# Kernel optimization log

Hardware: AMD Instinct MI355X
Metric: run time of the kernel (lower is better)

## Reference

```python
import jax, jax.numpy as jnp
import numpy as np

B, T, IN, H, L = 256, 80, 39, 256, 5


def _xavier(key, shape):
    fan_out, fan_in = shape[0], shape[1]
    std = (2.0 / (fan_in + fan_out)) ** 0.5
    return std * jax.random.normal(key, shape, dtype=jnp.float32)


def setup_inputs() -> dict:
    key = jax.random.key(0)
    ks = jax.random.split(key, 4 + 2 * L)
    x = jax.random.normal(ks[0], (B, T, IN), dtype=jnp.float32)
    # PyTorch LSTM params, gate order (i, f, g, o); biases zero per init.
    W_ih0 = _xavier(ks[1], (4 * H, IN))                       # layer 0 input weights
    W_ih_rest = jnp.stack([_xavier(ks[2 + l], (4 * H, H)) for l in range(L - 1)])  # [L-1,4H,H]
    W_hh = jnp.stack([_xavier(ks[1 + L + l], (4 * H, H)) for l in range(L)])       # [L,4H,H]
    b_ih = jnp.zeros((L, 4 * H), dtype=jnp.float32)
    b_hh = jnp.zeros((L, 4 * H), dtype=jnp.float32)
    fc_w = _xavier(ks[2 * L + 1], (1, H))
    fc_b = jnp.zeros((1,), dtype=jnp.float32)
    return {"x": x, "W_ih0": W_ih0, "W_ih_rest": W_ih_rest, "W_hh": W_hh,
            "b_ih": b_ih, "b_hh": b_hh, "fc_w": fc_w, "fc_b": fc_b}


def _lstm_layer(xs, W_ih, W_hh_l, b_ih_l, b_hh_l):
    # xs: [B,T,D]. Precompute input projection for all timesteps (one big GEMM).
    x_proj = jnp.einsum('btd,gd->btg', xs, W_ih) + b_ih_l + b_hh_l  # [B,T,4H]

    def step(carry, xp):
        h, c = carry
        gates = xp + h @ W_hh_l.T                 # [B,4H]
        i, f, g, o = jnp.split(gates, 4, axis=-1)
        c = jax.nn.sigmoid(f) * c + jax.nn.sigmoid(i) * jnp.tanh(g)
        h = jax.nn.sigmoid(o) * jnp.tanh(c)
        return (h, c), h

    b = xs.shape[0]
    h0 = jnp.zeros((b, H), dtype=xs.dtype)
    _, hs = jax.lax.scan(step, (h0, h0), jnp.swapaxes(x_proj, 0, 1))
    return jnp.swapaxes(hs, 0, 1)  # [B,T,H]


def reference(x, W_ih0, W_ih_rest, W_hh, b_ih, b_hh, fc_w, fc_b):
    h = _lstm_layer(x, W_ih0, W_hh[0], b_ih[0], b_hh[0])
    for l in range(1, L):
        h = _lstm_layer(h, W_ih_rest[l - 1], W_hh[l], b_ih[l], b_hh[l])
    out = jnp.einsum('bth,oh->bto', h, fc_w) + fc_b  # [B,T,1]
    return out[..., 0]  # [B,T]
```

## Files before the change

kernel.cpp:

```cpp
#include <hip/hip_runtime.h>

#define B_ 256
#define T_ 80
#define IN_ 39
#define H_ 256
#define G_ 1024
#define L_ 5
#define TC_ 16
#define NCH_ 5

#define XP_FLOATS   (B_ * TC_ * G_)
#define HBUF_FLOATS (B_ * T_ * H_)
#define CBUF_FLOATS (B_ * H_)
#define WG_FLOATS   (L_ * G_ * H_)
#define HX_FLOATS   (2 * 32 * 2048)
#define FLG_INTS_L  2048

#define AG __HIP_MEMORY_SCOPE_AGENT
#define WGS __HIP_MEMORY_SCOPE_WORKGROUP

__device__ __forceinline__ float sigm(float x) { return 1.0f / (1.0f + expf(-x)); }
__device__ __forceinline__ void fma4(float4& a, float s, const float4& w) {
    a.x = fmaf(s, w.x, a.x); a.y = fmaf(s, w.y, a.y);
    a.z = fmaf(s, w.z, a.z); a.w = fmaf(s, w.w, a.w);
}
__device__ __forceinline__ void red4(float4& a) {
    a.x += __shfl_xor(a.x, 32); a.y += __shfl_xor(a.y, 32);
    a.z += __shfl_xor(a.z, 32); a.w += __shfl_xor(a.w, 32);
}

__device__ __forceinline__ float4 ld_mall_16B(const float* p) {
    float4 v;
    asm volatile("global_load_dwordx4 %0, %1, off sc0 sc1\n\t"
                 "s_waitcnt vmcnt(0)"
                 : "=&v"(v) : "v"(p) : "memory");
    return v;
}

__device__ __forceinline__ void cbar(int* cnt, int& seq) {
    seq += 4;
    asm volatile("s_waitcnt lgkmcnt(0)" ::: "memory");
    if ((threadIdx.x & 63) == 0)
        __hip_atomic_fetch_add(cnt, 1, __ATOMIC_RELAXED, WGS);
    while (__hip_atomic_load(cnt, __ATOMIC_RELAXED, WGS) < seq)
        __builtin_amdgcn_s_sleep(1);
    asm volatile("s_waitcnt lgkmcnt(0)" ::: "memory");
}

extern "C" __global__ void __launch_bounds__(256)
wt_kernel(const float* __restrict__ Whh, float* __restrict__ Wg) {
    const int gid = blockIdx.x * 256 + threadIdx.x;
    const int g4 = gid & 3;
    const int j  = (gid >> 2) & 31;
    const int k  = (gid >> 7) & 255;
    const int s  = (gid >> 15) & 7;
    const int l  = gid >> 18;
    Wg[gid] = Whh[((size_t)(l * 1024 + g4 * 256 + s * 32 + j)) * 256 + k];
}

extern "C" __global__ void __launch_bounds__(256)
proj_multi(const float* __restrict__ x, const float* __restrict__ Wih0,
           const float* __restrict__ Wihr,
           const float* __restrict__ bih, const float* __restrict__ bhh,
           const float* __restrict__ hbuf,
           float* __restrict__ xp_base, unsigned long long xp_s,
           int d, int lmin) {
    __shared__ float As[16 * 132];
    __shared__ float Bs[16 * 68];
    const int task = blockIdx.x >> 9;
    const int l = lmin + task;
    const int ch = d - l;
    const int t0 = ch * TC_;
    const int K = (l == 0) ? IN_ : H_;
    const float* src = (l == 0) ? x : hbuf;
    const float* Wih = (l == 0) ? Wih0 : (Wihr + (size_t)(l - 1) * G_ * H_);
    const float* bihl = bih + l * G_;
    const float* bhhl = bhh + l * G_;
    float* xp = xp_base + (size_t)l * xp_s;

    const int bid9 = blockIdx.x & 511;
    const int tid = threadIdx.x;
    const int mt = bid9 >> 4, nt = bid9 & 15;
    const int tx = tid & 15, ty = tid >> 4;
    const int lrA = tid >> 1, lc8 = (tid & 1) * 8;
    const int lrB = tid >> 2, lc4 = (tid & 3) * 4;

    const int ar = mt * 128 + lrA;
    const int ab = ar >> 4;
    const int at = t0 + (ar & 15);
    const float* arow = src + ((size_t)ab * T_ + at) * K;
    const int brow_idx = (lrB & 3) * 256 + nt * 16 + (lrB >> 2);
    const float* brow = Wih + (size_t)brow_idx * K;

    float acc[8][4];
    #pragma unroll
    for (int i = 0; i < 8; ++i)
        #pragma unroll
        for (int j = 0; j < 4; ++j) acc[i][j] = 0.0f;

    for (int k0 = 0; k0 < K; k0 += 16) {
        __syncthreads();
        if (K == IN_) {
            #pragma unroll
            for (int i = 0; i < 8; ++i) {
                const int k = k0 + lc8 + i;
                As[(lc8 + i) * 132 + lrA] = (k < IN_) ? arow[k] : 0.0f;
            }
            #pragma unroll
            for (int i = 0; i < 4; ++i) {
                const int k = k0 + lc4 + i;
                Bs[(lc4 + i) * 68 + lrB] = (k < IN_) ? brow[k] : 0.0f;
            }
        } else {
            float4 a0 = *(const float4*)(arow + k0 + lc8);
            float4 a1 = *(const float4*)(arow + k0 + lc8 + 4);
            As[(lc8 + 0) * 132 + lrA] = a0.x;
            As[(lc8 + 1) * 132 + lrA] = a0.y;
            As[(lc8 + 2) * 132 + lrA] = a0.z;
            As[(lc8 + 3) * 132 + lrA] = a0.w;
            As[(lc8 + 4) * 132 + lrA] = a1.x;
            As[(lc8 + 5) * 132 + lrA] = a1.y;
            As[(lc8 + 6) * 132 + lrA] = a1.z;
            As[(lc8 + 7) * 132 + lrA] = a1.w;
            float4 bv = *(const float4*)(brow + k0 + lc4);
            Bs[(lc4 + 0) * 68 + lrB] = bv.x;
            Bs[(lc4 + 1) * 68 + lrB] = bv.y;
            Bs[(lc4 + 2) * 68 + lrB] = bv.z;
            Bs[(lc4 + 3) * 68 + lrB] = bv.w;
        }
        __syncthreads();
        #pragma unroll
        for (int kk = 0; kk < 16; ++kk) {
            const float4 aA = *(const float4*)&As[kk * 132 + ty * 8];
            const float4 aB = *(const float4*)&As[kk * 132 + ty * 8 + 4];
            const float4 b4 = *(const float4*)&Bs[kk * 68 + tx * 4];
            acc[0][0] += aA.x * b4.x; acc[0][1] += aA.x * b4.y;
            acc[0][2] += aA.x * b4.z; acc[0][3] += aA.x * b4.w;
            acc[1][0] += aA.y * b4.x; acc[1][1] += aA.y * b4.y;
            acc[1][2] += aA.y * b4.z; acc[1][3] += aA.y * b4.w;
            acc[2][0] += aA.z * b4.x; acc[2][1] += aA.z * b4.y;
            acc[2][2] += aA.z * b4.z; acc[2][3] += aA.z * b4.w;
            acc[3][0] += aA.w * b4.x; acc[3][1] += aA.w * b4.y;
            acc[3][2] += aA.w * b4.z; acc[3][3] += aA.w * b4.w;
            acc[4][0] += aB.x * b4.x; acc[4][1] += aB.x * b4.y;
            acc[4][2] += aB.x * b4.z; acc[4][3] += aB.x * b4.w;
            acc[5][0] += aB.y * b4.x; acc[5][1] += aB.y * b4.y;
            acc[5][2] += aB.y * b4.z; acc[5][3] += aB.y * b4.w;
            acc[6][0] += aB.z * b4.x; acc[6][1] += aB.z * b4.y;
            acc[6][2] += aB.z * b4.z; acc[6][3] += aB.z * b4.w;
            acc[7][0] += aB.w * b4.x; acc[7][1] += aB.w * b4.y;
            acc[7][2] += aB.w * b4.z; acc[7][3] += aB.w * b4.w;
        }
    }
    const int unit = nt * 16 + tx;
    const float bs0 = bihl[0 * 256 + unit] + bhhl[0 * 256 + unit];
    const float bs1 = bihl[1 * 256 + unit] + bhhl[1 * 256 + unit];
    const float bs2 = bihl[2 * 256 + unit] + bhhl[2 * 256 + unit];
    const float bs3 = bihl[3 * 256 + unit] + bhhl[3 * 256 + unit];
    #pragma unroll
    for (int i = 0; i < 8; ++i) {
        const int row = mt * 128 + ty * 8 + i;
        float4 o;
        o.x = acc[i][0] + bs0; o.y = acc[i][1] + bs1;
        o.z = acc[i][2] + bs2; o.w = acc[i][3] + bs3;
        *(float4*)&xp[(size_t)row * G_ + unit * 4] = o;
    }
}

extern "C" __global__ void __launch_bounds__(512, 2)
rec_multi(const float* __restrict__ xp_base, unsigned long long xp_s,
          const float* __restrict__ wg, float* __restrict__ hbuf,
          float* __restrict__ cbuf_base, unsigned long long cb_s,
          float* __restrict__ hx_base, unsigned long long hx_s,
          int* __restrict__ flg_base, unsigned long long flg_s,
          int d, int lmin) {
    __shared__ float sH[2048];
    __shared__ float sP[2 * 4 * 32 * 20];
    __shared__ int   barC[2];

    const int tid = threadIdx.x;
    const int task = blockIdx.x >> 8;
    const int l = lmin + task;
    const int ch = d - l;
    const int b8 = blockIdx.x & 255;
    const int grp = b8 >> 3;
    const int s   = b8 & 7;
    const int t0 = ch * TC_;
    const int chkb = (l * NCH_ + ch) * TC_;
    const int first = (ch == 0);

    const float* xp = xp_base + (size_t)l * xp_s;
    const float* Wg_l = wg + (size_t)l * (G_ * H_);
    float* cbuf = cbuf_base + (size_t)l * cb_s;
    float* hx = hx_base + (size_t)l * hx_s;
    int* flg = flg_base + (size_t)l * flg_s;

    const int c = tid >> 8;
    const int tp = tid & 255;
    const int jj = tp & 31;
    const int ks = tp >> 5;
    const int w4 = tp >> 6;
    const int fb2 = tp >> 5;
    const int unit = s * 32 + jj;
    const int bglob = grp * 8 + c * 4 + (fb2 & 3);
    float* sPc = sP + c * 2560;
    int* mycnt = barC + c;
    int* flgc = flg + (grp * 2 + c) * 32;

    if (tid < 2) barC[tid] = 0;

    const float4* Wg4 = (const float4*)Wg_l + (size_t)s * 8192;
    float4 wreg[32];
    #pragma unroll
    for (int kk = 0; kk < 32; ++kk)
        wreg[kk] = Wg4[(size_t)(ks * 32 + kk) * 32 + jj];

    float creg = 0.0f;
    if (tp < 128 && !first) creg = cbuf[(size_t)bglob * H_ + unit];

    __syncthreads();

    const float4* sH4 = (const float4*)sH;
    int seq = 0;

    for (int tt = 0; tt < TC_; ++tt) {
        const int t = t0 + tt;

        float4 xv = make_float4(0.f, 0.f, 0.f, 0.f);
        if (tp < 128)
            xv = *(const float4*)&xp[((size_t)bglob * TC_ + tt) * G_ + unit * 4];

        if (tt == 0 && first) {
            *(float4*)&sH[tp * 8 + c * 4] = make_float4(0.f, 0.f, 0.f, 0.f);
        } else {
            if ((tid & 63) < 8) {
                int* fp = flgc + (tid & 63);
                const int tgt = chkb + tt;
                while (__hip_atomic_load(fp, __ATOMIC_RELAXED, AG) < tgt)
                    __builtin_amdgcn_s_sleep(1);
            }
            const float* hsf = hx + (size_t)((((tt + 1) & 1)) * 32 + grp) * 2048
                                  + (size_t)tp * 8 + c * 4;
            *(float4*)&sH[tp * 8 + c * 4] = ld_mall_16B(hsf);
        }
        cbar(mycnt, seq);

        float4 a0 = {0,0,0,0}, a1 = {0,0,0,0}, a2 = {0,0,0,0}, a3 = {0,0,0,0};
        #pragma unroll
        for (int kk = 0; kk < 32; ++kk) {
            const int k = ks * 32 + kk;
            const float4 wv = wreg[kk];
            const float4 hc = sH4[k * 2 + c];
            fma4(a0, hc.x, wv); fma4(a1, hc.y, wv);
            fma4(a2, hc.z, wv); fma4(a3, hc.w, wv);
        }
        red4(a0); red4(a1); red4(a2); red4(a3);
        if ((tid & 63) < 32) {
            float4* pp = (float4*)&sPc[(w4 * 32 + jj) * 20];
            pp[0] = a0; pp[1] = a1; pp[2] = a2; pp[3] = a3;
        }
        cbar(mycnt, seq);

        if (tp < 128) {
            float4 g4 = xv;
            #pragma unroll
            for (int w2 = 0; w2 < 4; ++w2) {
                const float4 pw = *(const float4*)&sPc[(w2 * 32 + jj) * 20 + fb2 * 4];
                g4.x += pw.x; g4.y += pw.y; g4.z += pw.z; g4.w += pw.w;
            }
            const float I = sigm(g4.x);
            const float F = sigm(g4.y);
            const float Gt = tanhf(g4.z);
            const float O = sigm(g4.w);
            creg = F * creg + I * Gt;
            const float hval = O * tanhf(creg);
            hbuf[((size_t)bglob * T_ + t) * H_ + unit] = hval;

            const float hpart = __shfl_xor(hval, 32);
            if ((fb2 & 1) == 0) {
                const unsigned long long pv =
                    ((unsigned long long)__float_as_uint(hpart) << 32)
                    | __float_as_uint(hval);
                unsigned long long* dst = (unsigned long long*)
                    (hx + (size_t)((tt & 1) * 32 + grp) * 2048
                        + unit * 8 + c * 4 + fb2);
                __hip_atomic_store(dst, pv, __ATOMIC_RELAXED, AG);
            }
        }

        asm volatile("s_waitcnt vmcnt(0)" ::: "memory");
        cbar(mycnt, seq);
        if (tp == 0)
            __hip_atomic_store(flgc + s, chkb + tt + 1, __ATOMIC_RELAXED, AG);
    }

    if (tp < 128) cbuf[(size_t)bglob * H_ + unit] = creg;
}

extern "C" __global__ void __launch_bounds__(128)
fc_kernel(const float* __restrict__ hbuf, const float* __restrict__ fcw,
          const float* __restrict__ fcb, float* __restrict__ out) {
    __shared__ float wsm[256];
    const int tid = threadIdx.x;
    const int b = blockIdx.x;
    if (tid < 64) ((float4*)wsm)[tid] = ((const float4*)fcw)[tid];
    __syncthreads();
    if (tid < T_) {
        const float4* h4p = (const float4*)(hbuf + ((size_t)b * T_ + tid) * H_);
        const float4* w4p = (const float4*)wsm;
        float acc = fcb[0];
        #pragma unroll 8
        for (int k4 = 0; k4 < 64; ++k4) {
            float4 h4 = h4p[k4], w4 = w4p[k4];
            acc += h4.x * w4.x + h4.y * w4.y + h4.z * w4.z + h4.w * w4.w;
        }
        out[b * T_ + tid] = acc;
    }
}

extern "C" void kernel_launch(void* const* d_in, const int* in_sizes, int n_in,
                              void* d_out, int out_size, void* d_ws, size_t ws_size,
                              hipStream_t stream) {
    (void)in_sizes; (void)n_in; (void)out_size;
    const float* x    = (const float*)d_in[0];
    const float* Wih0 = (const float*)d_in[1];
    const float* Wihr = (const float*)d_in[2];
    const float* Whh  = (const float*)d_in[3];
    const float* bih  = (const float*)d_in[4];
    const float* bhh  = (const float*)d_in[5];
    const float* fcw  = (const float*)d_in[6];
    const float* fcb  = (const float*)d_in[7];
    float* out = (float*)d_out;
    float* ws  = (float*)d_ws;

    const size_t WF_ELEMS = (size_t)5 * XP_FLOATS + HBUF_FLOATS
                          + (size_t)5 * CBUF_FLOATS + WG_FLOATS
                          + (size_t)5 * HX_FLOATS + (size_t)5 * FLG_INTS_L;
    const int wf = (ws_size >= WF_ELEMS * 4) ? 1 : 0;

    const unsigned long long xp_s  = wf ? XP_FLOATS   : 0;
    const unsigned long long cb_s  = wf ? CBUF_FLOATS : 0;
    const unsigned long long hx_s  = wf ? HX_FLOATS   : 0;
    const unsigned long long flg_s = wf ? FLG_INTS_L  : 0;
    const int nrep = wf ? 5 : 1;

    float* xp   = ws;
    float* hbuf = xp + (size_t)nrep * XP_FLOATS;
    float* cbuf = hbuf + HBUF_FLOATS;
    float* wg   = cbuf + (size_t)nrep * CBUF_FLOATS;
    float* hx   = wg + WG_FLOATS;
    int*   flg  = (int*)(hx + (size_t)nrep * HX_FLOATS);

    hipMemsetAsync(flg, 0, (size_t)nrep * FLG_INTS_L * sizeof(int), stream);
    hipLaunchKernelGGL(wt_kernel, dim3(WG_FLOATS / 256), dim3(256), 0, stream, Whh, wg);

    if (wf) {
        for (int dd = 0; dd <= L_ + NCH_ - 2; ++dd) {
            const int lmin = (dd - (NCH_ - 1) > 0) ? (dd - (NCH_ - 1)) : 0;
            const int lmax = (dd < L_ - 1) ? dd : (L_ - 1);
            const int n = lmax - lmin + 1;
            hipLaunchKernelGGL(proj_multi, dim3(n * 512), dim3(256), 0, stream,
                               x, Wih0, Wihr, bih, bhh, hbuf, xp, xp_s, dd, lmin);
            hipLaunchKernelGGL(rec_multi, dim3(n * 256), dim3(512), 0, stream,
                               xp, xp_s, wg, hbuf, cbuf, cb_s, hx, hx_s,
                               flg, flg_s, dd, lmin);
        }
    } else {
        for (int l = 0; l < L_; ++l) {
            for (int ch = 0; ch < NCH_; ++ch) {
                const int dd = l + ch;
                hipLaunchKernelGGL(proj_multi, dim3(512), dim3(256), 0, stream,
                                   x, Wih0, Wihr, bih, bhh, hbuf, xp, xp_s, dd, l);
                hipLaunchKernelGGL(rec_multi, dim3(256), dim3(512), 0, stream,
                                   xp, xp_s, wg, hbuf, cbuf, cb_s, hx, hx_s,
                                   flg, flg_s, dd, l);
            }
        }
    }
    hipLaunchKernelGGL(fc_kernel, dim3(B_), dim3(128), 0, stream, hbuf, fcw, fcb, out);
}
```

Measured before the change: 2.172 ms.

## Replace diagonal wavefront with fixed two-task-per-launch layer/chunk schedule

The multi-layer wavefront used to launch every ready (layer, chunk) task on a diagonal together, up to five tasks and 1280 recurrence blocks at once. It now follows a hand-written 14-step schedule that launches at most two tasks per projection/recurrence pair, so at most 512 recurrence blocks. That fits two 512-thread blocks per CU under the launch bounds. The aim is to keep all blocks that spin-wait on each other co-resident and to stop five tasks from fighting over the CUs. The cost is more serial launches than the nine-diagonal critical path, and correctness now depends on the hand-ordered schedule respecting the layer and chunk dependencies.

```diff
diff --git a/kernel.cpp b/kernel.cpp
--- a/kernel.cpp
+++ b/kernel.cpp
@@ -59,17 +59,17 @@
 }
 
 extern "C" __global__ void __launch_bounds__(256)
-proj_multi(const float* __restrict__ x, const float* __restrict__ Wih0,
-           const float* __restrict__ Wihr,
-           const float* __restrict__ bih, const float* __restrict__ bhh,
-           const float* __restrict__ hbuf,
-           float* __restrict__ xp_base, unsigned long long xp_s,
-           int d, int lmin) {
+proj_pair(const float* __restrict__ x, const float* __restrict__ Wih0,
+          const float* __restrict__ Wihr,
+          const float* __restrict__ bih, const float* __restrict__ bhh,
+          const float* __restrict__ hbuf,
+          float* __restrict__ xp_base, unsigned long long xp_s,
+          int l0, int ch0, int l1, int ch1) {
     __shared__ float As[16 * 132];
     __shared__ float Bs[16 * 68];
     const int task = blockIdx.x >> 9;
-    const int l = lmin + task;
-    const int ch = d - l;
+    const int l  = task ? l1 : l0;
+    const int ch = task ? ch1 : ch0;
     const int t0 = ch * TC_;
     const int K = (l == 0) ? IN_ : H_;
     const float* src = (l == 0) ? x : hbuf;
@@ -168,20 +168,20 @@
 }
 
 extern "C" __global__ void __launch_bounds__(512, 2)
-rec_multi(const float* __restrict__ xp_base, unsigned long long xp_s,
-          const float* __restrict__ wg, float* __restrict__ hbuf,
-          float* __restrict__ cbuf_base, unsigned long long cb_s,
-          float* __restrict__ hx_base, unsigned long long hx_s,
-          int* __restrict__ flg_base, unsigned long long flg_s,
-          int d, int lmin) {
+rec_pair(const float* __restrict__ xp_base, unsigned long long xp_s,
+         const float* __restrict__ wg, float* __restrict__ hbuf,
+         float* __restrict__ cbuf_base, unsigned long long cb_s,
+         float* __restrict__ hx_base, unsigned long long hx_s,
+         int* __restrict__ flg_base, unsigned long long flg_s,
+         int l0, int ch0, int l1, int ch1) {
     __shared__ float sH[2048];
     __shared__ float sP[2 * 4 * 32 * 20];
     __shared__ int   barC[2];
 
     const int tid = threadIdx.x;
     const int task = blockIdx.x >> 8;
-    const int l = lmin + task;
-    const int ch = d - l;
+    const int l  = task ? l1 : l0;
+    const int ch = task ? ch1 : ch0;
     const int b8 = blockIdx.x & 255;
     const int grp = b8 >> 3;
     const int s   = b8 & 7;
@@ -355,25 +355,31 @@
     hipLaunchKernelGGL(wt_kernel, dim3(WG_FLOATS / 256), dim3(256), 0, stream, Whh, wg);
 
     if (wf) {
-        for (int dd = 0; dd <= L_ + NCH_ - 2; ++dd) {
-            const int lmin = (dd - (NCH_ - 1) > 0) ? (dd - (NCH_ - 1)) : 0;
-            const int lmax = (dd < L_ - 1) ? dd : (L_ - 1);
-            const int n = lmax - lmin + 1;
-            hipLaunchKernelGGL(proj_multi, dim3(n * 512), dim3(256), 0, stream,
-                               x, Wih0, Wihr, bih, bhh, hbuf, xp, xp_s, dd, lmin);
-            hipLaunchKernelGGL(rec_multi, dim3(n * 256), dim3(512), 0, stream,
+        static const int sched[14][4] = {
+            {0,0,-1,-1}, {1,0, 0,1}, {2,0, 1,1}, {0,2, 3,0}, {2,1, 1,2},
+            {0,3, 4,0}, {3,1, 2,2}, {1,3, 0,4}, {4,1, 3,2}, {2,3, 1,4},
+            {4,2, 3,3}, {4,3, 2,4}, {3,4,-1,-1}, {4,4,-1,-1},
+        };
+        for (int si = 0; si < 14; ++si) {
+            const int l0 = sched[si][0], c0 = sched[si][1];
+            const int l1 = sched[si][2], c1 = sched[si][3];
+            const int n = (l1 >= 0) ? 2 : 1;
+            hipLaunchKernelGGL(proj_pair, dim3(n * 512), dim3(256), 0, stream,
+                               x, Wih0, Wihr, bih, bhh, hbuf, xp, xp_s,
+                               l0, c0, l1, c1);
+            hipLaunchKernelGGL(rec_pair, dim3(n * 256), dim3(512), 0, stream,
                                xp, xp_s, wg, hbuf, cbuf, cb_s, hx, hx_s,
-                               flg, flg_s, dd, lmin);
+                               flg, flg_s, l0, c0, l1, c1);
         }
     } else {
         for (int l = 0; l < L_; ++l) {
             for (int ch = 0; ch < NCH_; ++ch) {
-                const int dd = l + ch;
-                hipLaunchKernelGGL(proj_multi, dim3(512), dim3(256), 0, stream,
-                                   x, Wih0, Wihr, bih, bhh, hbuf, xp, xp_s, dd, l);
-                hipLaunchKernelGGL(rec_multi, dim3(256), dim3(512), 0, stream,
+                hipLaunchKernelGGL(proj_pair, dim3(512), dim3(256), 0, stream,
+                                   x, Wih0, Wihr, bih, bhh, hbuf, xp, xp_s,
+                                   l, ch, -1, -1);
+                hipLaunchKernelGGL(rec_pair, dim3(256), dim3(512), 0, stream,
                                    xp, xp_s, wg, hbuf, cbuf, cb_s, hx, hx_s,
-                                   flg, flg_s, dd, l);
+                                   flg, flg_s, l, ch, -1, -1);
             }
         }
     }
```

Measured after the change: 2.231 ms. +2.7%, slower.
